# Optimization experiments

Measured on AMD Instinct MI355X. Metric: run time of the kernel, lower is better.

## Reference

```python
import jax, jax.numpy as jnp
import numpy as np

B_SZ = 8
D_MODEL = 512
D_STATE = 64
N2 = D_STATE // 2  # S4D uses complex-conjugate pairs -> d_state//2 complex modes
L_SEQ = 2048


def setup_inputs() -> dict:
    key = jax.random.key(0)
    ks = jax.random.split(key, 16)
    d = D_MODEL
    scale = 1.0 / np.sqrt(d)
    inp = {
        "x": jax.random.normal(ks[0], (B_SZ, d, L_SEQ), dtype=jnp.float32),
        # q/k/v projections (nn.Linear: weight (out,in), bias (out,))
        "Wq": jax.random.normal(ks[1], (d, d), dtype=jnp.float32) * scale,
        "bq": jax.random.normal(ks[2], (d,), dtype=jnp.float32) * scale,
        "Wk": jax.random.normal(ks[3], (d, d), dtype=jnp.float32) * scale,
        "bk": jax.random.normal(ks[4], (d,), dtype=jnp.float32) * scale,
        "Wv": jax.random.normal(ks[5], (d, d), dtype=jnp.float32) * scale,
        "bv": jax.random.normal(ks[6], (d,), dtype=jnp.float32) * scale,
        # Shift layer params
        "shift_C": jax.random.normal(ks[7], (1, d, D_STATE), dtype=jnp.float32),
        "shift_D": jax.random.normal(ks[8], (d,), dtype=jnp.float32),
        # S4D (diagonal SSM) params
        "log_dt": jax.random.uniform(ks[9], (d,), dtype=jnp.float32,
                                      minval=np.log(1e-3), maxval=np.log(1e-1)),
        "A_real": jnp.log(0.5 * jnp.ones((d, N2), dtype=jnp.float32)),
        "A_imag": jnp.broadcast_to(np.pi * jnp.arange(N2, dtype=jnp.float32), (d, N2)),
        "C_re": jax.random.normal(ks[10], (d, N2), dtype=jnp.float32) * np.sqrt(0.5),
        "C_im": jax.random.normal(ks[11], (d, N2), dtype=jnp.float32) * np.sqrt(0.5),
        "s4_D": jax.random.normal(ks[12], (d,), dtype=jnp.float32),
    }
    return inp


def _linear_chan(x, W, b):
    # x: (B, H, L); Linear applied over channel dim H -> (B, H_out, L)
    return jnp.einsum("bhl,dh->bdl", x, W) + b[:, None]


def _shift(u, C, Dp):
    """Shift SSM: causal conv with kernel = first L taps of C (computed via FFT
    exactly as the torch source does). u: (B, H, L)."""
    L = u.shape[-1]
    n = 2 * L
    H, S = C.shape[1], C.shape[2]
    Bmat = jnp.zeros((H, S), dtype=u.dtype).at[:, 0].set(1.0)
    B_fc = jnp.conj(jnp.fft.rfft(Bmat, n=n, axis=-1))  # (H, L+1)
    C_f = jnp.fft.rfft(C, n=n, axis=-1)                # (1, H, L+1)
    kernel = jnp.fft.irfft(B_fc * C_f, n=n, axis=-1)[..., :L]  # (1, H, L)
    kernel_f = jnp.fft.rfft(kernel, n=n, axis=-1)      # (1, H, L+1)
    u_f = jnp.fft.rfft(u, n=n, axis=-1)                # (B, H, L+1)
    y = jnp.fft.irfft(u_f * kernel_f, n=n, axis=-1)[..., :L]
    return y + u * Dp[:, None]


def _s4d(u, log_dt, A_real, A_imag, C_re, C_im, Dp):
    """Standard S4D forward: ZOH-discretized diagonal SSM kernel + FFT conv.
    u: (B, H, L)."""
    L = u.shape[-1]
    n = 2 * L
    dt = jnp.exp(log_dt)[:, None]                  # (H, 1)
    A = -jnp.exp(A_real) + 1j * A_imag             # (H, N2)
    dtA = A * dt                                   # (H, N2)
    C = (C_re + 1j * C_im) * (jnp.exp(dtA) - 1.0) / A
    vand = jnp.exp(dtA[:, :, None] * jnp.arange(L))  # (H, N2, L)
    K = 2.0 * jnp.einsum("hn,hnl->hl", C, vand).real  # (H, L)
    y = jnp.fft.irfft(jnp.fft.rfft(u, n=n, axis=-1) * jnp.fft.rfft(K, n=n, axis=-1),
                      n=n, axis=-1)[..., :L]
    return y + u * Dp[:, None]


def reference(x, Wq, bq, Wk, bk, Wv, bv, shift_C, shift_D,
              log_dt, A_real, A_imag, C_re, C_im, s4_D):
    q = _linear_chan(x, Wq, bq)
    k = _linear_chan(x, Wk, bk)
    v = _linear_chan(x, Wv, bv)
    shift_out = _shift(k, shift_C, shift_D)
    s4d_out = _s4d(v * shift_out, log_dt, A_real, A_imag, C_re, C_im, s4_D)
    return q * s4d_out
```

## Files before the change

kernel.cpp:

```cpp
#include <hip/hip_runtime.h>
#include <cstdint>


#define BATCH 8
#define DMODEL 512
#define LSEQ 2048

typedef _Float16 half_t;
typedef __attribute__((ext_vector_type(4))) _Float16 half4v;
typedef __attribute__((ext_vector_type(8))) _Float16 half8v;
typedef __attribute__((ext_vector_type(4))) float floatx4;

__device__ __forceinline__ void gload_lds16(const half_t* g, half_t* l) {
  __builtin_amdgcn_global_load_lds(
      (const __attribute__((address_space(1))) uint32_t*)g,
      (__attribute__((address_space(3))) uint32_t*)l, 16, 0, 0);
}

__global__ __launch_bounds__(256) void convert_w(
    const float* __restrict__ Wq, const float* __restrict__ Wk,
    const float* __restrict__ Wv, half_t* __restrict__ W16) {
  int i = blockIdx.x * 256 + threadIdx.x;
  const float* src = (i < 262144) ? Wq : ((i < 524288) ? Wk : Wv);
  int j = i & 262143;
  W16[i] = (half_t)src[j];
}

__global__ __launch_bounds__(256) void transpose_x(
    const float* __restrict__ x, half_t* __restrict__ xT) {
  __shared__ float tile[32][33];
  int b = blockIdx.z;
  int d0 = blockIdx.y * 32;
  int l0 = blockIdx.x * 32;
  int tx = threadIdx.x, ty = threadIdx.y;
  const float* xp = x + (size_t)b * DMODEL * LSEQ;
#pragma unroll
  for (int k = 0; k < 4; k++)
    tile[ty + 8 * k][tx] = xp[(size_t)(d0 + ty + 8 * k) * LSEQ + l0 + tx];
  __syncthreads();
  half_t* op = xT + (size_t)b * LSEQ * DMODEL;
#pragma unroll
  for (int k = 0; k < 4; k++)
    op[(size_t)(l0 + ty + 8 * k) * DMODEL + d0 + tx] = (half_t)tile[tx][ty + 8 * k];
}

__global__ __launch_bounds__(256) void s4d_setup(
    const float* __restrict__ log_dt, const float* __restrict__ A_real,
    const float* __restrict__ A_imag, const float* __restrict__ C_re,
    const float* __restrict__ C_im, float* __restrict__ mc) {
  int i = blockIdx.x * 256 + threadIdx.x;
  int h = i >> 5;
  float dt = expf(log_dt[h]);
  float Ar = -expf(A_real[i]);
  float Ai = A_imag[i];
  float a = dt * Ar, b = dt * Ai;
  float ea = expf(a);
  float wr = ea * cosf(b), wi = ea * sinf(b);
  float Am2 = Ar * Ar + Ai * Ai;
  float zr = wr - 1.0f, zi = wi;
  float qr = (zr * Ar + zi * Ai) / Am2;
  float qi = (zi * Ar - zr * Ai) / Am2;
  float cr = C_re[i] * qr - C_im[i] * qi;
  float ci = C_re[i] * qi + C_im[i] * qr;
  float e64 = expf(64.0f * a);
  float wTr = e64 * cosf(64.0f * b), wTi = e64 * sinf(64.0f * b);
  mc[0 * 16384 + i] = a;   mc[1 * 16384 + i] = b;
  mc[2 * 16384 + i] = wr;  mc[3 * 16384 + i] = wi;
  mc[4 * 16384 + i] = cr;  mc[5 * 16384 + i] = ci;
  mc[6 * 16384 + i] = wTr; mc[7 * 16384 + i] = wTi;
}

__global__ __launch_bounds__(256) void s4d_tables(
    const float* __restrict__ mc, const float* __restrict__ shC,
    half_t* __restrict__ Vt, half_t* __restrict__ Et, half_t* __restrict__ Tt,
    half_t* __restrict__ T1t, half_t* __restrict__ T2t) {
  __shared__ float Kt[64];
  __shared__ float tapl[64];
  int h = blockIdx.x;
  int tid = threadIdx.x;
  if (tid < 64) { Kt[tid] = 0.f; tapl[tid] = shC[h * 64 + tid]; }
  __syncthreads();
  size_t base = (size_t)h * 4096;
  {
    int r = tid >> 2;
    int nb = (tid & 3) * 8;
    float ksum = 0.f;
#pragma unroll
    for (int i = 0; i < 8; i++) {
      int n = nb + i, hn = h * 32 + n;
      float a = mc[hn], b = mc[16384 + hn];
      float cr = mc[4 * 16384 + hn], ci = mc[5 * 16384 + hn];
      float er = expf(a * (float)r);
      float w0r = er * cosf(b * (float)r), w0i = er * sinf(b * (float)r);
      ksum += 2.f * (cr * w0r - ci * w0i);
      float wr = mc[2 * 16384 + hn], wi = mc[3 * 16384 + hn];
      float w1r = w0r * wr - w0i * wi, w1i = w0r * wi + w0i * wr;
      Et[base + r * 64 + 2 * n]     = (half_t)(2.f * (cr * w1r - ci * w1i));
      Et[base + r * 64 + 2 * n + 1] = (half_t)(-2.f * (cr * w1i + ci * w1r));
      Vt[base + (2 * n) * 64 + (63 - r)]     = (half_t)w0r;
      Vt[base + (2 * n + 1) * 64 + (63 - r)] = (half_t)w0i;
    }
    atomicAdd(&Kt[r], ksum);
  }
  __syncthreads();
#pragma unroll
  for (int e = 0; e < 16; e++) {
    int idx = e * 256 + tid;
    int r = idx >> 6, t = idx & 63;
    int d = r - t;
    Tt[base + idx]  = (d >= 0) ? (half_t)Kt[d] : (half_t)0.f;
    T1t[base + idx] = (d >= 0) ? (half_t)tapl[d] : (half_t)0.f;
    T2t[base + idx] = (d < 0) ? (half_t)tapl[64 + d] : (half_t)0.f;
  }
}

__global__ __launch_bounds__(256) void gemm_qkv(
    const half_t* __restrict__ xT, const half_t* __restrict__ Wstk,
    const float* __restrict__ bq, const float* __restrict__ bk,
    const float* __restrict__ bv, half_t* __restrict__ outq,
    half_t* __restrict__ outk, half_t* __restrict__ outv) {
  __shared__ half_t As[128 * 64];
  __shared__ half_t Bs[128 * 64];
  int flat = blockIdx.x;
  int swz = (flat & 7) * 192 + (flat >> 3);
  int nt = swz / 12, mt = swz - nt * 12;
  int n0 = nt * 128, m0 = mt * 128;
  int tid = threadIdx.x;
  int lane = tid & 63, wid = tid >> 6;
  int wr = wid >> 1, wc = wid & 1;
  int lrow = lane & 15, lg = lane >> 4;
  int rsub = lane >> 3, ssub = lane & 7;
  int gslot = ssub ^ rsub;

  floatx4 acc[4][4];
#pragma unroll
  for (int i = 0; i < 4; i++)
#pragma unroll
    for (int j = 0; j < 4; j++) acc[i][j] = (floatx4){0.f, 0.f, 0.f, 0.f};

  const half_t* gA = Wstk + (size_t)(m0 + wid * 32 + rsub) * 512 + gslot * 8;
  const half_t* gB = xT + (size_t)(n0 + wid * 32 + rsub) * 512 + gslot * 8;

  for (int kk = 0; kk < 512; kk += 64) {
#pragma unroll
    for (int i = 0; i < 4; i++) {
      int c = wid * 4 + i;
      gload_lds16(gA + (size_t)i * 8 * 512 + kk, As + c * 512);
      gload_lds16(gB + (size_t)i * 8 * 512 + kk, Bs + c * 512);
    }
    __syncthreads();
#pragma unroll
    for (int h = 0; h < 2; h++) {
      half8v af[4], bf[4];
#pragma unroll
      for (int i = 0; i < 4; i++) {
        int r = wr * 64 + i * 16 + lrow;
        int s = (h * 4 + lg) ^ (r & 7);
        af[i] = *(const half8v*)(As + r * 64 + s * 8);
      }
#pragma unroll
      for (int j = 0; j < 4; j++) {
        int r = wc * 64 + j * 16 + lrow;
        int s = (h * 4 + lg) ^ (r & 7);
        bf[j] = *(const half8v*)(Bs + r * 64 + s * 8);
      }
#pragma unroll
      for (int i = 0; i < 4; i++)
#pragma unroll
        for (int j = 0; j < 4; j++)
          acc[i][j] = __builtin_amdgcn_mfma_f32_16x16x32_f16(af[i], bf[j],
                                                             acc[i][j], 0, 0, 0);
    }
    __syncthreads();
  }
#pragma unroll
  for (int i = 0; i < 4; i++) {
    int dd = m0 + wr * 64 + i * 16 + 4 * lg;
    int z = dd >> 9;
    const float* bias = (z == 0) ? bq : ((z == 1) ? bk : bv);
    half_t* outp = (z == 0) ? outq : ((z == 1) ? outk : outv);
    int d = dd & 511;
#pragma unroll
    for (int j = 0; j < 4; j++) {
      int n = n0 + wc * 64 + j * 16 + lrow;
      int b = n >> 11, l = n & 2047;
#pragma unroll
      for (int reg = 0; reg < 4; reg++)
        outp[((size_t)(b * 512 + d + reg)) * 2048 + l] =
            (half_t)(acc[i][j][reg] + bias[d + reg]);
    }
  }
}

__global__ __launch_bounds__(256) void s4d_main(
    const half_t* __restrict__ kbuf, const half_t* __restrict__ vbuf,
    const half_t* __restrict__ Vt, const half_t* __restrict__ Et,
    const half_t* __restrict__ Tt, const half_t* __restrict__ T1t,
    const half_t* __restrict__ T2t, const float* __restrict__ mc,
    const float* __restrict__ shD, const float* __restrict__ s4D,
    const half_t* __restrict__ qbuf, float* __restrict__ outp) {
  __shared__ half_t kl[33 * 72];
  __shared__ half_t vg[32 * 72];
  __shared__ half_t uh[32 * 72];
  __shared__ half_t tab0[64 * 72];
  __shared__ half_t tab1[64 * 72];
  __shared__ half_t tab2[64 * 72];
  __shared__ float SG[32 * 66];
  int bh = blockIdx.x;
  int h = bh & 511;
  int tid = threadIdx.x;
  int lane = tid & 63, wid = tid >> 6;
  int lrow = lane & 15, lg = lane >> 4;
  int mi = wid & 1;
  int ri0 = wid >> 1;

  if (tid < 9) {
    half8v zz = {(_Float16)0, (_Float16)0, (_Float16)0, (_Float16)0,
                 (_Float16)0, (_Float16)0, (_Float16)0, (_Float16)0};
    *(half8v*)(kl + tid * 8) = zz;
  }
  {
    int sj = tid >> 3, sc = (tid & 7) * 8;
    const half_t* kp = kbuf + (size_t)bh * 2048;
    const half_t* vp = vbuf + (size_t)bh * 2048;
    *(half8v*)(kl + (1 + sj) * 72 + sc) = *(const half8v*)(kp + sj * 64 + sc);
    *(half8v*)(vg + sj * 72 + sc) = *(const half8v*)(vp + sj * 64 + sc);
  }
  {
    size_t tb = (size_t)h * 4096;
#pragma unroll
    for (int e = 0; e < 2; e++) {
      int idx = e * 2048 + tid * 8;
      int r = idx >> 6, c = idx & 63;
      *(half8v*)(tab0 + r * 72 + c) = *(const half8v*)(T1t + tb + idx);
      *(half8v*)(tab1 + r * 72 + c) = *(const half8v*)(T2t + tb + idx);
      *(half8v*)(tab2 + r * 72 + c) = *(const half8v*)(Vt + tb + idx);
    }
  }
  float sDsh = shD[h];
  float sD4 = s4D[h];
  __syncthreads();

  floatx4 acc[2];
  acc[0] = (floatx4){0.f, 0.f, 0.f, 0.f};
  acc[1] = (floatx4){0.f, 0.f, 0.f, 0.f};
#pragma unroll
  for (int ks = 0; ks < 4; ks++) {
    int ko = ks * 16 + 4 * lg;
    half4v a1 = *(const half4v*)(kl + (1 + mi * 16 + lrow) * 72 + ko);
    half4v a2 = *(const half4v*)(kl + (mi * 16 + lrow) * 72 + ko);
#pragma unroll
    for (int tt = 0; tt < 2; tt++) {
      int ri = ri0 + tt * 2;
      half4v b1 = *(const half4v*)(tab0 + (ri * 16 + lrow) * 72 + ko);
      half4v b2 = *(const half4v*)(tab1 + (ri * 16 + lrow) * 72 + ko);
      acc[tt] = __builtin_amdgcn_mfma_f32_16x16x16f16(a1, b1, acc[tt], 0, 0, 0);
      acc[tt] = __builtin_amdgcn_mfma_f32_16x16x16f16(a2, b2, acc[tt], 0, 0, 0);
    }
  }
#pragma unroll
  for (int tt = 0; tt < 2; tt++) {
    int ri = ri0 + tt * 2;
#pragma unroll
    for (int reg = 0; reg < 4; reg++) {
      int j = mi * 16 + 4 * lg + reg;
      int r = ri * 16 + lrow;
      float kvv = (float)kl[(1 + j) * 72 + r];
      float vvv = (float)vg[j * 72 + r];
      uh[j * 72 + r] = (half_t)(vvv * (acc[tt][reg] + sDsh * kvv));
    }
  }
  __syncthreads();

  acc[0] = (floatx4){0.f, 0.f, 0.f, 0.f};
  acc[1] = (floatx4){0.f, 0.f, 0.f, 0.f};
#pragma unroll
  for (int ks = 0; ks < 4; ks++) {
    int ko = ks * 16 + 4 * lg;
    half4v a = *(const half4v*)(uh + (mi * 16 + lrow) * 72 + ko);
#pragma unroll
    for (int tt = 0; tt < 2; tt++) {
      int ri = ri0 + tt * 2;
      half4v b = *(const half4v*)(tab2 + (ri * 16 + lrow) * 72 + ko);
      acc[tt] = __builtin_amdgcn_mfma_f32_16x16x16f16(a, b, acc[tt], 0, 0, 0);
    }
  }
#pragma unroll
  for (int tt = 0; tt < 2; tt++) {
    int ri = ri0 + tt * 2;
#pragma unroll
    for (int reg = 0; reg < 4; reg++) {
      int j = mi * 16 + 4 * lg + reg;
      SG[j * 66 + ri * 16 + lrow] = acc[tt][reg];
    }
  }
  __syncthreads();

  if (tid < 32) {
    int n = tid, hn = h * 32 + n;
    float wTr = mc[6 * 16384 + hn], wTi = mc[7 * 16384 + hn];
    float gr = 0.f, gi = 0.f;
    for (int j = 0; j < 32; j++) {
      float tr = SG[j * 66 + 2 * n], ti = SG[j * 66 + 2 * n + 1];
      SG[j * 66 + 2 * n] = gr; SG[j * 66 + 2 * n + 1] = gi;
      float nr = wTr * gr - wTi * gi + tr;
      gi = wTr * gi + wTi * gr + ti;
      gr = nr;
    }
  }
  {
    size_t tb = (size_t)h * 4096;
#pragma unroll
    for (int e = 0; e < 2; e++) {
      int idx = e * 2048 + tid * 8;
      int r = idx >> 6, c = idx & 63;
      *(half8v*)(tab0 + r * 72 + c) = *(const half8v*)(Et + tb + idx);
      *(half8v*)(tab1 + r * 72 + c) = *(const half8v*)(Tt + tb + idx);
    }
  }
  __syncthreads();

  {
    int j = tid >> 3, m0 = (tid & 7) * 8;
    half8v g;
#pragma unroll
    for (int i = 0; i < 8; i++) g[i] = (half_t)SG[j * 66 + m0 + i];
    *(half8v*)(vg + j * 72 + m0) = g;
  }
  __syncthreads();

  acc[0] = (floatx4){0.f, 0.f, 0.f, 0.f};
  acc[1] = (floatx4){0.f, 0.f, 0.f, 0.f};
#pragma unroll
  for (int ks = 0; ks < 4; ks++) {
    int ko = ks * 16 + 4 * lg;
    half4v ag = *(const half4v*)(vg + (mi * 16 + lrow) * 72 + ko);
    half4v au = *(const half4v*)(uh + (mi * 16 + lrow) * 72 + ko);
#pragma unroll
    for (int tt = 0; tt < 2; tt++) {
      int ri = ri0 + tt * 2;
      half4v be = *(const half4v*)(tab0 + (ri * 16 + lrow) * 72 + ko);
      half4v bt = *(const half4v*)(tab1 + (ri * 16 + lrow) * 72 + ko);
      acc[tt] = __builtin_amdgcn_mfma_f32_16x16x16f16(ag, be, acc[tt], 0, 0, 0);
      acc[tt] = __builtin_amdgcn_mfma_f32_16x16x16f16(au, bt, acc[tt], 0, 0, 0);
    }
  }
  const half_t* qp = qbuf + (size_t)bh * 2048;
  float* op = outp + (size_t)bh * 2048;
#pragma unroll
  for (int tt = 0; tt < 2; tt++) {
    int ri = ri0 + tt * 2;
#pragma unroll
    for (int reg = 0; reg < 4; reg++) {
      int j = mi * 16 + 4 * lg + reg;
      int r = ri * 16 + lrow;
      int l = j * 64 + r;
      float y = acc[tt][reg] + sD4 * (float)uh[j * 72 + r];
      op[l] = (float)qp[l] * y;
    }
  }
}

extern "C" void kernel_launch(void* const* d_in, const int* in_sizes, int n_in,
                              void* d_out, int out_size, void* d_ws, size_t ws_size,
                              hipStream_t stream) {
  const float* x      = (const float*)d_in[0];
  const float* Wq     = (const float*)d_in[1];
  const float* bq     = (const float*)d_in[2];
  const float* Wk     = (const float*)d_in[3];
  const float* bk     = (const float*)d_in[4];
  const float* Wv     = (const float*)d_in[5];
  const float* bv     = (const float*)d_in[6];
  const float* shC    = (const float*)d_in[7];
  const float* shD    = (const float*)d_in[8];
  const float* log_dt = (const float*)d_in[9];
  const float* A_real = (const float*)d_in[10];
  const float* A_imag = (const float*)d_in[11];
  const float* C_re   = (const float*)d_in[12];
  const float* C_im   = (const float*)d_in[13];
  const float* s4D    = (const float*)d_in[14];
  float* out = (float*)d_out;
  half_t* wsh = (half_t*)d_ws;

  half_t* qbuf = wsh;
  half_t* kbuf = wsh + 8388608;
  half_t* vbuf = wsh + 16777216;
  half_t* xT16 = wsh + 25165824;
  half_t* W16  = wsh + 33554432;
  half_t* Vt   = wsh + 34340864;
  half_t* Et   = wsh + 36438016;
  half_t* Tt   = wsh + 38535168;
  half_t* T1t  = wsh + 40632320;
  half_t* T2t  = wsh + 42729472;
  float*  mc   = (float*)(wsh + 44826624);

  convert_w<<<3072, 256, 0, stream>>>(Wq, Wk, Wv, W16);
  transpose_x<<<dim3(64, 16, 8), dim3(32, 8), 0, stream>>>(x, xT16);
  s4d_setup<<<64, 256, 0, stream>>>(log_dt, A_real, A_imag, C_re, C_im, mc);
  s4d_tables<<<512, 256, 0, stream>>>(mc, shC, Vt, Et, Tt, T1t, T2t);
  gemm_qkv<<<dim3(1536), 256, 0, stream>>>(xT16, W16, bq, bk, bv,
                                           qbuf, kbuf, vbuf);
  s4d_main<<<4096, 256, 0, stream>>>(kbuf, vbuf, Vt, Et, Tt, T1t, T2t,
                                     mc, shD, s4D, qbuf, out);
}
```

Baseline: 101.0 us.

## Pre-swizzle tables and k/v images for direct LDS loads, double-buffer QKV GEMM

Tables and the k/v GEMM outputs are now written in global memory already in an XOR-swizzled 64-column layout. This lets s4d_main stage them straight into LDS with global_load_lds and read them as 8-wide fragments for 16x16x32 MFMAs, instead of padded 72-stride copies. The QKV GEMM switches to a double-buffered 32-deep K pipeline, and s4d_setup is merged into s4d_tables. The Et/Tt reload is issued earlier so it overlaps the second phase. The swizzle conventions must match exactly across several kernels, which adds a correctness risk.

New measurement: 96.53 us. 4.4% less time.

```diff
diff --git a/kernel.cpp b/kernel.cpp
--- a/kernel.cpp
+++ b/kernel.cpp
@@ -2,7 +2,6 @@
 #include <cstdint>
 
 
-#define BATCH 8
 #define DMODEL 512
 #define LSEQ 2048
 
@@ -10,6 +9,8 @@
 typedef __attribute__((ext_vector_type(4))) _Float16 half4v;
 typedef __attribute__((ext_vector_type(8))) _Float16 half8v;
 typedef __attribute__((ext_vector_type(4))) float floatx4;
+
+#define SW(R, c) ((R) * 64 + ((((c) >> 3) ^ ((R) & 7)) << 3) + ((c) & 7))
 
 __device__ __forceinline__ void gload_lds16(const half_t* g, half_t* l) {
   __builtin_amdgcn_global_load_lds(
@@ -44,41 +45,36 @@
     op[(size_t)(l0 + ty + 8 * k) * DMODEL + d0 + tx] = (half_t)tile[tx][ty + 8 * k];
 }
 
-__global__ __launch_bounds__(256) void s4d_setup(
+__global__ __launch_bounds__(256) void s4d_tables(
     const float* __restrict__ log_dt, const float* __restrict__ A_real,
     const float* __restrict__ A_imag, const float* __restrict__ C_re,
-    const float* __restrict__ C_im, float* __restrict__ mc) {
-  int i = blockIdx.x * 256 + threadIdx.x;
-  int h = i >> 5;
-  float dt = expf(log_dt[h]);
-  float Ar = -expf(A_real[i]);
-  float Ai = A_imag[i];
-  float a = dt * Ar, b = dt * Ai;
-  float ea = expf(a);
-  float wr = ea * cosf(b), wi = ea * sinf(b);
-  float Am2 = Ar * Ar + Ai * Ai;
-  float zr = wr - 1.0f, zi = wi;
-  float qr = (zr * Ar + zi * Ai) / Am2;
-  float qi = (zi * Ar - zr * Ai) / Am2;
-  float cr = C_re[i] * qr - C_im[i] * qi;
-  float ci = C_re[i] * qi + C_im[i] * qr;
-  float e64 = expf(64.0f * a);
-  float wTr = e64 * cosf(64.0f * b), wTi = e64 * sinf(64.0f * b);
-  mc[0 * 16384 + i] = a;   mc[1 * 16384 + i] = b;
-  mc[2 * 16384 + i] = wr;  mc[3 * 16384 + i] = wi;
-  mc[4 * 16384 + i] = cr;  mc[5 * 16384 + i] = ci;
-  mc[6 * 16384 + i] = wTr; mc[7 * 16384 + i] = wTi;
-}
-
-__global__ __launch_bounds__(256) void s4d_tables(
-    const float* __restrict__ mc, const float* __restrict__ shC,
+    const float* __restrict__ C_im, const float* __restrict__ shC,
     half_t* __restrict__ Vt, half_t* __restrict__ Et, half_t* __restrict__ Tt,
-    half_t* __restrict__ T1t, half_t* __restrict__ T2t) {
-  __shared__ float Kt[64];
-  __shared__ float tapl[64];
+    half_t* __restrict__ T1t, half_t* __restrict__ T2t,
+    float* __restrict__ wt2) {
+  __shared__ float aL[32], bL[32], wrL[32], wiL[32], crL[32], ciL[32];
+  __shared__ float Kt[64], tapl[64];
   int h = blockIdx.x;
   int tid = threadIdx.x;
   if (tid < 64) { Kt[tid] = 0.f; tapl[tid] = shC[h * 64 + tid]; }
+  if (tid < 32) {
+    int n = tid, hn = h * 32 + n;
+    float dt = expf(log_dt[h]);
+    float Ar = -expf(A_real[hn]), Ai = A_imag[hn];
+    float a = dt * Ar, b = dt * Ai;
+    float ea = expf(a);
+    float wr = ea * cosf(b), wi = ea * sinf(b);
+    float Am2 = Ar * Ar + Ai * Ai;
+    float zr = wr - 1.0f, zi = wi;
+    float qr = (zr * Ar + zi * Ai) / Am2;
+    float qi = (zi * Ar - zr * Ai) / Am2;
+    aL[n] = a; bL[n] = b; wrL[n] = wr; wiL[n] = wi;
+    crL[n] = C_re[hn] * qr - C_im[hn] * qi;
+    ciL[n] = C_re[hn] * qi + C_im[hn] * qr;
+    float e64 = expf(64.0f * a);
+    wt2[h * 64 + 2 * n]     = e64 * cosf(64.0f * b);
+    wt2[h * 64 + 2 * n + 1] = e64 * sinf(64.0f * b);
+  }
   __syncthreads();
   size_t base = (size_t)h * 4096;
   {
@@ -87,18 +83,18 @@
     float ksum = 0.f;
 #pragma unroll
     for (int i = 0; i < 8; i++) {
-      int n = nb + i, hn = h * 32 + n;
-      float a = mc[hn], b = mc[16384 + hn];
-      float cr = mc[4 * 16384 + hn], ci = mc[5 * 16384 + hn];
+      int n = nb + i;
+      float a = aL[n], b = bL[n];
+      float cr = crL[n], ci = ciL[n];
       float er = expf(a * (float)r);
       float w0r = er * cosf(b * (float)r), w0i = er * sinf(b * (float)r);
       ksum += 2.f * (cr * w0r - ci * w0i);
-      float wr = mc[2 * 16384 + hn], wi = mc[3 * 16384 + hn];
+      float wr = wrL[n], wi = wiL[n];
       float w1r = w0r * wr - w0i * wi, w1i = w0r * wi + w0i * wr;
-      Et[base + r * 64 + 2 * n]     = (half_t)(2.f * (cr * w1r - ci * w1i));
-      Et[base + r * 64 + 2 * n + 1] = (half_t)(-2.f * (cr * w1i + ci * w1r));
-      Vt[base + (2 * n) * 64 + (63 - r)]     = (half_t)w0r;
-      Vt[base + (2 * n + 1) * 64 + (63 - r)] = (half_t)w0i;
+      Et[base + SW(r, 2 * n)]     = (half_t)(2.f * (cr * w1r - ci * w1i));
+      Et[base + SW(r, 2 * n + 1)] = (half_t)(-2.f * (cr * w1i + ci * w1r));
+      Vt[base + SW(2 * n, 63 - r)]     = (half_t)w0r;
+      Vt[base + SW(2 * n + 1, 63 - r)] = (half_t)w0i;
     }
     atomicAdd(&Kt[r], ksum);
   }
@@ -108,9 +104,10 @@
     int idx = e * 256 + tid;
     int r = idx >> 6, t = idx & 63;
     int d = r - t;
-    Tt[base + idx]  = (d >= 0) ? (half_t)Kt[d] : (half_t)0.f;
-    T1t[base + idx] = (d >= 0) ? (half_t)tapl[d] : (half_t)0.f;
-    T2t[base + idx] = (d < 0) ? (half_t)tapl[64 + d] : (half_t)0.f;
+    size_t a = base + SW(r, t);
+    Tt[a]  = (d >= 0) ? (half_t)Kt[d] : (half_t)0.f;
+    T1t[a] = (d >= 0) ? (half_t)tapl[d] : (half_t)0.f;
+    T2t[a] = (d < 0) ? (half_t)tapl[64 + d] : (half_t)0.f;
   }
 }
 
@@ -119,8 +116,8 @@
     const float* __restrict__ bq, const float* __restrict__ bk,
     const float* __restrict__ bv, half_t* __restrict__ outq,
     half_t* __restrict__ outk, half_t* __restrict__ outv) {
-  __shared__ half_t As[128 * 64];
-  __shared__ half_t Bs[128 * 64];
+  __shared__ half_t As[2][128 * 32];
+  __shared__ half_t Bs[2][128 * 32];
   int flat = blockIdx.x;
   int swz = (flat & 7) * 192 + (flat >> 3);
   int nt = swz / 12, mt = swz - nt * 12;
@@ -129,8 +126,7 @@
   int lane = tid & 63, wid = tid >> 6;
   int wr = wid >> 1, wc = wid & 1;
   int lrow = lane & 15, lg = lane >> 4;
-  int rsub = lane >> 3, ssub = lane & 7;
-  int gslot = ssub ^ rsub;
+  int r_in = lane >> 2, s_in = lane & 3;
 
   floatx4 acc[4][4];
 #pragma unroll
@@ -138,73 +134,83 @@
 #pragma unroll
     for (int j = 0; j < 4; j++) acc[i][j] = (floatx4){0.f, 0.f, 0.f, 0.f};
 
-  const half_t* gA = Wstk + (size_t)(m0 + wid * 32 + rsub) * 512 + gslot * 8;
-  const half_t* gB = xT + (size_t)(n0 + wid * 32 + rsub) * 512 + gslot * 8;
-
-  for (int kk = 0; kk < 512; kk += 64) {
+  auto STAGE = [&](int buf, int kk) {
+#pragma unroll
+    for (int i = 0; i < 2; i++) {
+      int c = wid * 2 + i;
+      int row = c * 16 + r_in;
+      int ss = s_in ^ ((row >> 1) & 3);
+      gload_lds16(Wstk + (size_t)(m0 + row) * 512 + kk + ss * 8,
+                  &As[buf][c * 512]);
+      gload_lds16(xT + (size_t)(n0 + row) * 512 + kk + ss * 8,
+                  &Bs[buf][c * 512]);
+    }
+  };
+
+  STAGE(0, 0);
+  __syncthreads();
+  int cur = 0;
+  for (int t = 0; t < 16; t++) {
+    if (t < 15) STAGE(cur ^ 1, (t + 1) * 32);
+    half8v af[4], bf[4];
 #pragma unroll
     for (int i = 0; i < 4; i++) {
-      int c = wid * 4 + i;
-      gload_lds16(gA + (size_t)i * 8 * 512 + kk, As + c * 512);
-      gload_lds16(gB + (size_t)i * 8 * 512 + kk, Bs + c * 512);
-    }
+      int r = wr * 64 + i * 16 + lrow;
+      af[i] = *(const half8v*)(&As[cur][r * 32 + (lg ^ ((r >> 1) & 3)) * 8]);
+    }
+#pragma unroll
+    for (int j = 0; j < 4; j++) {
+      int r = wc * 64 + j * 16 + lrow;
+      bf[j] = *(const half8v*)(&Bs[cur][r * 32 + (lg ^ ((r >> 1) & 3)) * 8]);
+    }
+#pragma unroll
+    for (int i = 0; i < 4; i++)
+#pragma unroll
+      for (int j = 0; j < 4; j++)
+        acc[i][j] = __builtin_amdgcn_mfma_f32_16x16x32_f16(af[i], bf[j],
+                                                           acc[i][j], 0, 0, 0);
     __syncthreads();
-#pragma unroll
-    for (int h = 0; h < 2; h++) {
-      half8v af[4], bf[4];
-#pragma unroll
-      for (int i = 0; i < 4; i++) {
-        int r = wr * 64 + i * 16 + lrow;
-        int s = (h * 4 + lg) ^ (r & 7);
-        af[i] = *(const half8v*)(As + r * 64 + s * 8);
-      }
-#pragma unroll
-      for (int j = 0; j < 4; j++) {
-        int r = wc * 64 + j * 16 + lrow;
-        int s = (h * 4 + lg) ^ (r & 7);
-        bf[j] = *(const half8v*)(Bs + r * 64 + s * 8);
-      }
-#pragma unroll
-      for (int i = 0; i < 4; i++)
-#pragma unroll
-        for (int j = 0; j < 4; j++)
-          acc[i][j] = __builtin_amdgcn_mfma_f32_16x16x32_f16(af[i], bf[j],
-                                                             acc[i][j], 0, 0, 0);
-    }
-    __syncthreads();
-  }
+    cur ^= 1;
+  }
+
+  int z = m0 >> 9;
+  const float* bias = (z == 0) ? bq : ((z == 1) ? bk : bv);
+  half_t* outp = (z == 0) ? outq : ((z == 1) ? outk : outv);
 #pragma unroll
   for (int i = 0; i < 4; i++) {
-    int dd = m0 + wr * 64 + i * 16 + 4 * lg;
-    int z = dd >> 9;
-    const float* bias = (z == 0) ? bq : ((z == 1) ? bk : bv);
-    half_t* outp = (z == 0) ? outq : ((z == 1) ? outk : outv);
-    int d = dd & 511;
+    int d = (m0 + wr * 64 + i * 16 + 4 * lg) & 511;
 #pragma unroll
     for (int j = 0; j < 4; j++) {
       int n = n0 + wc * 64 + j * 16 + lrow;
       int b = n >> 11, l = n & 2047;
 #pragma unroll
-      for (int reg = 0; reg < 4; reg++)
-        outp[((size_t)(b * 512 + d + reg)) * 2048 + l] =
-            (half_t)(acc[i][j][reg] + bias[d + reg]);
+      for (int reg = 0; reg < 4; reg++) {
+        float val = acc[i][j][reg] + bias[d + reg];
+        size_t bhbase = ((size_t)(b * 512 + d + reg)) * 2048;
+        if (z == 0) {
+          outp[bhbase + l] = (half_t)val;
+        } else {
+          int jj = l >> 6, c = l & 63;
+          outp[bhbase + SW(jj, c)] = (half_t)val;
+        }
+      }
     }
   }
 }
 
 __global__ __launch_bounds__(256) void s4d_main(
-    const half_t* __restrict__ kbuf, const half_t* __restrict__ vbuf,
+    const half_t* __restrict__ kimg, const half_t* __restrict__ vimg,
+    const half_t* __restrict__ T1t, const half_t* __restrict__ T2t,
     const half_t* __restrict__ Vt, const half_t* __restrict__ Et,
-    const half_t* __restrict__ Tt, const half_t* __restrict__ T1t,
-    const half_t* __restrict__ T2t, const float* __restrict__ mc,
+    const half_t* __restrict__ Tt, const float* __restrict__ wt2,
     const float* __restrict__ shD, const float* __restrict__ s4D,
     const half_t* __restrict__ qbuf, float* __restrict__ outp) {
-  __shared__ half_t kl[33 * 72];
-  __shared__ half_t vg[32 * 72];
-  __shared__ half_t uh[32 * 72];
-  __shared__ half_t tab0[64 * 72];
-  __shared__ half_t tab1[64 * 72];
-  __shared__ half_t tab2[64 * 72];
+  __shared__ half_t kl[33 * 64];
+  __shared__ half_t vg[32 * 64];
+  __shared__ half_t uh[32 * 64];
+  __shared__ half_t tab0[64 * 64];
+  __shared__ half_t tab1[64 * 64];
+  __shared__ half_t tab2[64 * 64];
   __shared__ float SG[32 * 66];
   int bh = blockIdx.x;
   int h = bh & 511;
@@ -214,75 +220,86 @@
   int mi = wid & 1;
   int ri0 = wid >> 1;
 
-  if (tid < 9) {
+  {
+    const half_t* kp = kimg + (size_t)bh * 2048;
+    const half_t* vp = vimg + (size_t)bh * 2048;
+    size_t tb = (size_t)h * 4096;
+    gload_lds16(kp + wid * 512 + lane * 8, kl + 64 + wid * 512);
+    gload_lds16(vp + wid * 512 + lane * 8, vg + wid * 512);
+#pragma unroll
+    for (int i = 0; i < 2; i++) {
+      int c = wid * 2 + i;
+      gload_lds16(T1t + tb + c * 512 + lane * 8, tab0 + c * 512);
+      gload_lds16(T2t + tb + c * 512 + lane * 8, tab1 + c * 512);
+      gload_lds16(Vt + tb + c * 512 + lane * 8, tab2 + c * 512);
+    }
+  }
+  if (tid < 8) {
     half8v zz = {(_Float16)0, (_Float16)0, (_Float16)0, (_Float16)0,
                  (_Float16)0, (_Float16)0, (_Float16)0, (_Float16)0};
     *(half8v*)(kl + tid * 8) = zz;
   }
-  {
-    int sj = tid >> 3, sc = (tid & 7) * 8;
-    const half_t* kp = kbuf + (size_t)bh * 2048;
-    const half_t* vp = vbuf + (size_t)bh * 2048;
-    *(half8v*)(kl + (1 + sj) * 72 + sc) = *(const half8v*)(kp + sj * 64 + sc);
-    *(half8v*)(vg + sj * 72 + sc) = *(const half8v*)(vp + sj * 64 + sc);
-  }
-  {
-    size_t tb = (size_t)h * 4096;
-#pragma unroll
-    for (int e = 0; e < 2; e++) {
-      int idx = e * 2048 + tid * 8;
-      int r = idx >> 6, c = idx & 63;
-      *(half8v*)(tab0 + r * 72 + c) = *(const half8v*)(T1t + tb + idx);
-      *(half8v*)(tab1 + r * 72 + c) = *(const half8v*)(T2t + tb + idx);
-      *(half8v*)(tab2 + r * 72 + c) = *(const half8v*)(Vt + tb + idx);
-    }
-  }
   float sDsh = shD[h];
   float sD4 = s4D[h];
   __syncthreads();
+
+#define LDF(base, r, ks, key) \
+  (*(const half8v*)((base) + (r) * 64 + (((ks) * 4 + lg) ^ (key)) * 8))
 
   floatx4 acc[2];
   acc[0] = (floatx4){0.f, 0.f, 0.f, 0.f};
   acc[1] = (floatx4){0.f, 0.f, 0.f, 0.f};
-#pragma unroll
-  for (int ks = 0; ks < 4; ks++) {
-    int ko = ks * 16 + 4 * lg;
-    half4v a1 = *(const half4v*)(kl + (1 + mi * 16 + lrow) * 72 + ko);
-    half4v a2 = *(const half4v*)(kl + (mi * 16 + lrow) * 72 + ko);
-#pragma unroll
-    for (int tt = 0; tt < 2; tt++) {
-      int ri = ri0 + tt * 2;
-      half4v b1 = *(const half4v*)(tab0 + (ri * 16 + lrow) * 72 + ko);
-      half4v b2 = *(const half4v*)(tab1 + (ri * 16 + lrow) * 72 + ko);
-      acc[tt] = __builtin_amdgcn_mfma_f32_16x16x16f16(a1, b1, acc[tt], 0, 0, 0);
-      acc[tt] = __builtin_amdgcn_mfma_f32_16x16x16f16(a2, b2, acc[tt], 0, 0, 0);
+  {
+    int jA = mi * 16 + lrow;
+    int key1 = lrow & 7, key2 = (lrow + 7) & 7;
+#pragma unroll
+    for (int ks = 0; ks < 2; ks++) {
+      half8v a1 = LDF(kl, 1 + jA, ks, key1);
+      half8v a2 = LDF(kl, jA, ks, key2);
+#pragma unroll
+      for (int tt = 0; tt < 2; tt++) {
+        int rb = (ri0 + tt * 2) * 16 + lrow;
+        half8v b1 = LDF(tab0, rb, ks, lrow & 7);
+        half8v b2 = LDF(tab1, rb, ks, lrow & 7);
+        acc[tt] = __builtin_amdgcn_mfma_f32_16x16x32_f16(a1, b1, acc[tt], 0, 0, 0);
+        acc[tt] = __builtin_amdgcn_mfma_f32_16x16x32_f16(a2, b2, acc[tt], 0, 0, 0);
+      }
     }
   }
 #pragma unroll
   for (int tt = 0; tt < 2; tt++) {
-    int ri = ri0 + tt * 2;
 #pragma unroll
     for (int reg = 0; reg < 4; reg++) {
       int j = mi * 16 + 4 * lg + reg;
-      int r = ri * 16 + lrow;
-      float kvv = (float)kl[(1 + j) * 72 + r];
-      float vvv = (float)vg[j * 72 + r];
-      uh[j * 72 + r] = (half_t)(vvv * (acc[tt][reg] + sDsh * kvv));
-    }
-  }
-  __syncthreads();
+      int r = (ri0 + tt * 2) * 16 + lrow;
+      int cph = (((r >> 3) ^ (j & 7)) << 3) + (r & 7);
+      float kvv = (float)kl[(1 + j) * 64 + cph];
+      float vvv = (float)vg[j * 64 + cph];
+      uh[j * 64 + cph] = (half_t)(vvv * (acc[tt][reg] + sDsh * kvv));
+    }
+  }
+  __syncthreads();
+
+  {
+    size_t tb = (size_t)h * 4096;
+#pragma unroll
+    for (int i = 0; i < 2; i++) {
+      int c = wid * 2 + i;
+      gload_lds16(Et + tb + c * 512 + lane * 8, tab0 + c * 512);
+      gload_lds16(Tt + tb + c * 512 + lane * 8, tab1 + c * 512);
+    }
+  }
 
   acc[0] = (floatx4){0.f, 0.f, 0.f, 0.f};
   acc[1] = (floatx4){0.f, 0.f, 0.f, 0.f};
 #pragma unroll
-  for (int ks = 0; ks < 4; ks++) {
-    int ko = ks * 16 + 4 * lg;
-    half4v a = *(const half4v*)(uh + (mi * 16 + lrow) * 72 + ko);
+  for (int ks = 0; ks < 2; ks++) {
+    half8v a = LDF(uh, mi * 16 + lrow, ks, lrow & 7);
 #pragma unroll
     for (int tt = 0; tt < 2; tt++) {
-      int ri = ri0 + tt * 2;
-      half4v b = *(const half4v*)(tab2 + (ri * 16 + lrow) * 72 + ko);
-      acc[tt] = __builtin_amdgcn_mfma_f32_16x16x16f16(a, b, acc[tt], 0, 0, 0);
+      int rb = (ri0 + tt * 2) * 16 + lrow;
+      half8v b = LDF(tab2, rb, ks, lrow & 7);
+      acc[tt] = __builtin_amdgcn_mfma_f32_16x16x32_f16(a, b, acc[tt], 0, 0, 0);
     }
   }
 #pragma unroll
@@ -297,8 +314,8 @@
   __syncthreads();
 
   if (tid < 32) {
-    int n = tid, hn = h * 32 + n;
-    float wTr = mc[6 * 16384 + hn], wTi = mc[7 * 16384 + hn];
+    int n = tid;
+    float wTr = wt2[h * 64 + 2 * n], wTi = wt2[h * 64 + 2 * n + 1];
     float gr = 0.f, gi = 0.f;
     for (int j = 0; j < 32; j++) {
       float tr = SG[j * 66 + 2 * n], ti = SG[j * 66 + 2 * n + 1];
@@ -308,57 +325,47 @@
       gr = nr;
     }
   }
+  __syncthreads();
+
   {
-    size_t tb = (size_t)h * 4096;
-#pragma unroll
-    for (int e = 0; e < 2; e++) {
-      int idx = e * 2048 + tid * 8;
-      int r = idx >> 6, c = idx & 63;
-      *(half8v*)(tab0 + r * 72 + c) = *(const half8v*)(Et + tb + idx);
-      *(half8v*)(tab1 + r * 72 + c) = *(const half8v*)(Tt + tb + idx);
-    }
-  }
-  __syncthreads();
-
-  {
-    int j = tid >> 3, m0 = (tid & 7) * 8;
+    int j = tid >> 3, s = tid & 7;
     half8v g;
 #pragma unroll
-    for (int i = 0; i < 8; i++) g[i] = (half_t)SG[j * 66 + m0 + i];
-    *(half8v*)(vg + j * 72 + m0) = g;
+    for (int i = 0; i < 8; i++) g[i] = (half_t)SG[j * 66 + s * 8 + i];
+    *(half8v*)(vg + j * 64 + (s ^ (j & 7)) * 8) = g;
   }
   __syncthreads();
 
   acc[0] = (floatx4){0.f, 0.f, 0.f, 0.f};
   acc[1] = (floatx4){0.f, 0.f, 0.f, 0.f};
 #pragma unroll
-  for (int ks = 0; ks < 4; ks++) {
-    int ko = ks * 16 + 4 * lg;
-    half4v ag = *(const half4v*)(vg + (mi * 16 + lrow) * 72 + ko);
-    half4v au = *(const half4v*)(uh + (mi * 16 + lrow) * 72 + ko);
+  for (int ks = 0; ks < 2; ks++) {
+    half8v ag = LDF(vg, mi * 16 + lrow, ks, lrow & 7);
+    half8v au = LDF(uh, mi * 16 + lrow, ks, lrow & 7);
 #pragma unroll
     for (int tt = 0; tt < 2; tt++) {
-      int ri = ri0 + tt * 2;
-      half4v be = *(const half4v*)(tab0 + (ri * 16 + lrow) * 72 + ko);
-      half4v bt = *(const half4v*)(tab1 + (ri * 16 + lrow) * 72 + ko);
-      acc[tt] = __builtin_amdgcn_mfma_f32_16x16x16f16(ag, be, acc[tt], 0, 0, 0);
-      acc[tt] = __builtin_amdgcn_mfma_f32_16x16x16f16(au, bt, acc[tt], 0, 0, 0);
+      int rb = (ri0 + tt * 2) * 16 + lrow;
+      half8v be = LDF(tab0, rb, ks, lrow & 7);
+      half8v bt = LDF(tab1, rb, ks, lrow & 7);
+      acc[tt] = __builtin_amdgcn_mfma_f32_16x16x32_f16(ag, be, acc[tt], 0, 0, 0);
+      acc[tt] = __builtin_amdgcn_mfma_f32_16x16x32_f16(au, bt, acc[tt], 0, 0, 0);
     }
   }
   const half_t* qp = qbuf + (size_t)bh * 2048;
   float* op = outp + (size_t)bh * 2048;
 #pragma unroll
   for (int tt = 0; tt < 2; tt++) {
-    int ri = ri0 + tt * 2;
 #pragma unroll
     for (int reg = 0; reg < 4; reg++) {
       int j = mi * 16 + 4 * lg + reg;
-      int r = ri * 16 + lrow;
+      int r = (ri0 + tt * 2) * 16 + lrow;
+      int cph = (((r >> 3) ^ (j & 7)) << 3) + (r & 7);
+      float y = acc[tt][reg] + sD4 * (float)uh[j * 64 + cph];
       int l = j * 64 + r;
-      float y = acc[tt][reg] + sD4 * (float)uh[j * 72 + r];
       op[l] = (float)qp[l] * y;
     }
   }
+#undef LDF
 }
 
 extern "C" void kernel_launch(void* const* d_in, const int* in_sizes, int n_in,
@@ -392,14 +399,14 @@
   half_t* Tt   = wsh + 38535168;
   half_t* T1t  = wsh + 40632320;
   half_t* T2t  = wsh + 42729472;
-  float*  mc   = (float*)(wsh + 44826624);
+  float*  wt2  = (float*)(wsh + 44826624);
 
   convert_w<<<3072, 256, 0, stream>>>(Wq, Wk, Wv, W16);
   transpose_x<<<dim3(64, 16, 8), dim3(32, 8), 0, stream>>>(x, xT16);
-  s4d_setup<<<64, 256, 0, stream>>>(log_dt, A_real, A_imag, C_re, C_im, mc);
-  s4d_tables<<<512, 256, 0, stream>>>(mc, shC, Vt, Et, Tt, T1t, T2t);
+  s4d_tables<<<512, 256, 0, stream>>>(log_dt, A_real, A_imag, C_re, C_im, shC,
+                                      Vt, Et, Tt, T1t, T2t, wt2);
   gemm_qkv<<<dim3(1536), 256, 0, stream>>>(xT16, W16, bq, bk, bv,
                                            qbuf, kbuf, vbuf);
-  s4d_main<<<4096, 256, 0, stream>>>(kbuf, vbuf, Vt, Et, Tt, T1t, T2t,
-                                     mc, shD, s4D, qbuf, out);
-}
+  s4d_main<<<4096, 256, 0, stream>>>(kbuf, vbuf, T1t, T2t, Vt, Et, Tt,
+                                     wt2, shD, s4D, qbuf, out);
+}
```
